# Kernel tuning notes

Hardware: AMD Instinct MI355X
Metric: run time of the kernel (lower is better)

The kernel has to match this reference:

```python
import jax, jax.numpy as jnp
import numpy as np

NUM_LAYERS = 3
N = 4096
DIM = 512
TOPK = 8
BIG = 1.0e9
EPS_COS = 1e-8
EPS_NORM = 1e-12
BN_EPS = 1e-5
LAM_K = 64.0
LAM_Z = 16.0
SIGMA_INTRA = 0.99
ALPHA = np.linspace(1.0, 1.2, NUM_LAYERS)
BETA = np.linspace(0.0, 0.0, NUM_LAYERS)


def setup_inputs() -> dict:
    key = jax.random.key(0)
    ks = jax.random.split(key, 6)
    feats = jax.random.normal(ks[0], (NUM_LAYERS, N, DIM), dtype=jnp.float32)
    labels = jax.random.randint(ks[1], (N,), 0, 64, dtype=jnp.int64)
    fc1_w = jax.random.normal(ks[2], (NUM_LAYERS, DIM, DIM), dtype=jnp.float32) * (1.0 / np.sqrt(DIM))
    fc2_w = jax.random.normal(ks[3], (NUM_LAYERS, DIM, DIM), dtype=jnp.float32) * (1.0 / np.sqrt(DIM))
    bn_gamma = jnp.ones((NUM_LAYERS, DIM), dtype=jnp.float32)
    bn_beta = jnp.zeros((NUM_LAYERS, DIM), dtype=jnp.float32)
    proj_w = jax.random.normal(ks[4], (768, DIM), dtype=jnp.float32) * (1.0 / np.sqrt(DIM))
    return {"feats": feats, "labels": labels, "fc1_w": fc1_w, "fc2_w": fc2_w,
            "bn_gamma": bn_gamma, "bn_beta": bn_beta, "proj_w": proj_w}


def _l2norm(x, axis=-1):
    return x / jnp.maximum(jnp.linalg.norm(x, axis=axis, keepdims=True), EPS_NORM)


def _pairwise_cosine(G):
    Gn = _l2norm(G)
    sim = Gn @ Gn.T
    return jnp.clip(sim, -1.0 + EPS_COS, 1.0 - EPS_COS)


def _knn_mask(sim, base_mask, topk):
    n = sim.shape[0]
    masked = (sim - BIG * jnp.eye(n, dtype=sim.dtype)) * base_mask - (1.0 - base_mask) * BIG
    k = min(topk, max(n - 1, 1))
    idx = jax.lax.top_k(masked, k)[1]  # [N, k]
    st = jnp.zeros_like(sim).at[jnp.arange(n)[:, None], idx].set(1.0)
    return jnp.maximum(st, st.T)


def _build_intra_inter(sim, labels, topk):
    same = (labels[None, :] == labels[:, None]).astype(sim.dtype)
    diff = 1.0 - same
    m_intra = _knn_mask(sim, same, topk)
    m_inter = _knn_mask(sim, diff, topk)
    sim_intra = jnp.maximum(sim * m_intra, 0.0)
    sim_inter = jnp.maximum(sim * m_inter, 0.0)
    return sim_intra, sim_inter


def _normalize_sym(sim_graph, eps=1e-8):
    d = jnp.maximum(sim_graph.sum(axis=1), eps)
    dinv = d ** -0.5
    return dinv[:, None] * sim_graph * dinv[None, :]  # == diag(dinv) @ S @ diag(dinv)


def _diffusion(K, t_diff=1):
    out = K
    for _ in range(max(t_diff - 1, 0)):
        out = out @ K
    return out


def _bn_train(x, gamma, beta):
    m = x.mean(axis=0)
    v = x.var(axis=0)  # biased, as torch BN training
    return (x - m) / jnp.sqrt(v + BN_EPS) * gamma + beta


def _gam(S, G, w1, w2, gamma, beta):
    Z = S @ (G @ w1.T)
    Z = jax.nn.relu(_bn_train(Z, gamma, beta))
    Z = S @ (Z @ w2.T)
    return Z + G


def reference(feats, labels, fc1_w, fc2_w, bn_gamma, bn_beta, proj_w):
    n = feats.shape[1]
    eye = jnp.eye(n, dtype=feats.dtype)
    same = (labels[None, :] == labels[:, None]).astype(feats.dtype)

    K_list, Z_list = [], []
    for i in range(NUM_LAYERS):
        G = feats[i]
        sim = _pairwise_cosine(G)
        sim_intra, sim_inter = _build_intra_inter(sim, labels, TOPK)
        sim_graph = float(ALPHA[i]) * sim_intra + float(BETA[i]) * sim_inter + 1e-6 * eye
        S = _normalize_sym(sim_graph)
        K = _diffusion(S, t_diff=1)
        Z = _gam(S, G, fc1_w[i], fc2_w[i], bn_gamma[i], bn_beta[i])
        K_list.append(K)
        Z_list.append(Z)

    loss_K = jnp.zeros((), dtype=feats.dtype)
    loss_Z = jnp.zeros((), dtype=feats.dtype)
    for i in range(1, NUM_LAYERS):
        K_tgt = jax.lax.stop_gradient(K_list[i])
        loss_K = loss_K + jnp.mean((K_list[i - 1] - K_tgt) ** 2)
        Zp = _l2norm(Z_list[i - 1] @ proj_w.T)
        Zc = _l2norm(Z_list[i] @ proj_w.T)
        loss_Z = loss_Z + jnp.mean((Zp - jax.lax.stop_gradient(Zc)) ** 2)

    K_idea = _diffusion(same * SIGMA_INTRA, t_diff=1)
    loss_idea = jnp.mean((K_list[-1] - K_idea) ** 2)
    return LAM_K * loss_K + LAM_Z * loss_Z + loss_idea
```

## Files before the change

kernel.cpp:

```cpp
#include <hip/hip_runtime.h>
#include <math.h>
#include <stdint.h>

#define NROWS 4096
#define DIM   512
#define NCLS  64
#define CAP   128
#define PD    768
#define NL    3
#define PARTSZ (size_t)(NCLS * 2 * 1024)

typedef __attribute__((ext_vector_type(8))) short short8v;
typedef __attribute__((ext_vector_type(4))) float f32x4;

__device__ __forceinline__ unsigned short f2bf(float f) {
  unsigned u = __float_as_uint(f);
  unsigned r = (u + 0x7FFF + ((u >> 16) & 1)) >> 16;
  return (unsigned short)r;
}

__device__ __forceinline__ void gload_lds16(const void* g, void* l) {
  auto* lp = reinterpret_cast<__attribute__((address_space(3))) unsigned int*>(
      reinterpret_cast<uintptr_t>(l));
  const auto* gp = reinterpret_cast<const __attribute__((address_space(1))) unsigned int*>(
      reinterpret_cast<uintptr_t>(g));
  __builtin_amdgcn_global_load_lds(gp, lp, 16, 0, 0);
}

__device__ __forceinline__ float waveReduce(float v) {
#pragma unroll
  for (int o = 32; o > 0; o >>= 1) v += __shfl_down(v, o);
  return v;
}

__device__ __forceinline__ float blockReduce(float v) {
  __shared__ float sh[4];
  int lane = threadIdx.x & 63, wv = threadIdx.x >> 6;
  v = waveReduce(v);
  if (lane == 0) sh[wv] = v;
  __syncthreads();
  float t = 0.f;
  if (threadIdx.x == 0) {
    int nw = (blockDim.x + 63) >> 6;
    for (int i = 0; i < nw; ++i) t += sh[i];
  }
  return t;
}

__global__ __launch_bounds__(256) void k_hist(const int* __restrict__ labels, int* __restrict__ chunkCnt) {
  __shared__ int h[NCLS];
  int t = threadIdx.x;
  if (t < NCLS) h[t] = 0;
  __syncthreads();
  atomicAdd(&h[labels[blockIdx.x * 256 + t]], 1);
  __syncthreads();
  if (t < NCLS) chunkCnt[blockIdx.x * NCLS + t] = h[t];
}

__global__ void k_scan(const int* __restrict__ chunkCnt, int* __restrict__ cnt,
                       int* __restrict__ off, int* __restrict__ chunkBase, float* __restrict__ acc) {
  __shared__ int sc[NCLS];
  int c = threadIdx.x;
  if (c < 8) acc[c] = 0.f;
  int tot = 0;
  for (int b = 0; b < 16; ++b) tot += chunkCnt[b * NCLS + c];
  cnt[c] = tot;
  sc[c] = tot;
  __syncthreads();
  if (c == 0) {
    int s = 0;
    for (int i = 0; i < NCLS; ++i) { int tv = sc[i]; sc[i] = s; s += tv; }
  }
  __syncthreads();
  int run = sc[c];
  off[c] = run;
  for (int b = 0; b < 16; ++b) { chunkBase[b * NCLS + c] = run; run += chunkCnt[b * NCLS + c]; }
  if (c == 0) off[NCLS] = NROWS;
}

__global__ __launch_bounds__(256) void k_scatter(const int* __restrict__ labels, const int* __restrict__ chunkBase,
                                                 int* __restrict__ perm, int* __restrict__ clsp) {
  __shared__ int lab[256];
  int t = threadIdx.x;
  int r = blockIdx.x * 256 + t;
  int c = labels[r];
  lab[t] = c;
  __syncthreads();
  int rank = 0;
  for (int j = 0; j < t; ++j) rank += (lab[j] == c);
  int pos = chunkBase[blockIdx.x * NCLS + c] + rank;
  perm[pos] = r;
  clsp[pos] = c;
}

__global__ __launch_bounds__(128) void k_prepw(const float* __restrict__ feats, const int* __restrict__ perm,
                                               unsigned short* __restrict__ Gpb, float* __restrict__ invn,
                                               const float4* __restrict__ fc1, const float4* __restrict__ fc2,
                                               const float4* __restrict__ proj,
                                               ushort4* __restrict__ w1, ushort4* __restrict__ w2,
                                               ushort4* __restrict__ pj, float* __restrict__ rnorm) {
  int y = blockIdx.y;
  if (y == NL) {
    const int nW = NL * DIM * DIM / 4;
    const int nP = PD * DIM / 4;
    int idx = blockIdx.x * 128 + threadIdx.x;
    const float4* src; ushort4* dst; int k;
    if (idx < nW) { src = fc1; dst = w1; k = idx; }
    else if (idx < 2 * nW) { src = fc2; dst = w2; k = idx - nW; }
    else if (idx < 2 * nW + nP) { src = proj; dst = pj; k = idx - 2 * nW; }
    else {
      int z = idx - (2 * nW + nP);
      if (z < NL * NROWS) rnorm[z] = 0.f;
      return;
    }
    float4 v = src[k];
    ushort4 o;
    o.x = f2bf(v.x); o.y = f2bf(v.y); o.z = f2bf(v.z); o.w = f2bf(v.w);
    dst[k] = o;
    return;
  }
  __shared__ float red[2];
  int l = y;
  const float* G = feats + (size_t)l * NROWS * DIM;
  unsigned short* Gp = Gpb + (size_t)l * NROWS * DIM;
  int row = blockIdx.x, t = threadIdx.x;
  const float4* src = (const float4*)(G + (size_t)perm[row] * DIM);
  float4 v = src[t];
  ushort4 b;
  b.x = f2bf(v.x); b.y = f2bf(v.y); b.z = f2bf(v.z); b.w = f2bf(v.w);
  *(ushort4*)(Gp + (size_t)row * DIM + t * 4) = b;
  float ss = v.x * v.x + v.y * v.y + v.z * v.z + v.w * v.w;
  ss = waveReduce(ss);
  if ((t & 63) == 0) red[t >> 6] = ss;
  __syncthreads();
  if (t == 0) invn[l * NROWS + row] = 1.f / fmaxf(sqrtf(red[0] + red[1]), 1e-12f);
}

__global__ __launch_bounds__(256) void k_sim(const unsigned short* __restrict__ Gpb,
                                             const float* __restrict__ invn,
                                             const int* __restrict__ cnt, const int* __restrict__ off,
                                             float* __restrict__ sim) {
  int l = blockIdx.z;
  const unsigned short* Gp = Gpb + (size_t)l * NROWS * DIM;
  const float* inv = invn + (size_t)l * NROWS;
  float* sm = sim + (size_t)l * NCLS * CAP * CAP;
  int c = blockIdx.y;
  int n = min(cnt[c], CAP);
  int ti = blockIdx.x >> 2, tj = blockIdx.x & 3;
  if (ti * 32 >= n || tj * 32 >= n) return;
  int base = off[c];
  __shared__ short As[32][40];
  __shared__ short Bs[32][40];
  const int t = threadIdx.x;
  const int lane = t & 63, wv = t >> 6;
  const int qi = wv >> 1, qj = wv & 1;
  const int fr = lane & 15, kg = lane >> 4;
  const int half = t >> 7, tt = t & 127;
  const int srow = tt >> 2, scol = (tt & 3) * 8;
  int gr = (half ? tj : ti) * 32 + srow;
  const unsigned short* ps = Gp + (size_t)(base + min(gr, n - 1)) * DIM + scol;
  short* dst = half ? &Bs[srow][scol] : &As[srow][scol];
  f32x4 acc = {};
  for (int k0 = 0; k0 < DIM; k0 += 32) {
    short8v v = *(const short8v*)(ps + k0);
    __syncthreads();
    *(short8v*)dst = v;
    __syncthreads();
    short8v af = *(const short8v*)&As[qi * 16 + fr][kg * 8];
    short8v bf = *(const short8v*)&Bs[qj * 16 + fr][kg * 8];
    acc = __builtin_amdgcn_mfma_f32_16x16x32_bf16(af, bf, acc, 0, 0, 0);
  }
  int gj = tj * 32 + qj * 16 + fr;
  int r0 = ti * 32 + qi * 16 + kg * 4;
  if (gj < n) {
    float sj = inv[base + gj];
#pragma unroll
    for (int r = 0; r < 4; ++r) {
      int gi = r0 + r;
      if (gi < n) {
        float v = acc[r] * inv[base + gi] * sj;
        v = fminf(fmaxf(v, -1.0f + 1e-8f), 1.0f - 1e-8f);
        sm[((size_t)c * CAP + gi) * CAP + gj] = v;
      }
    }
  }
}

__global__ __launch_bounds__(256) void k_topk(const float* __restrict__ sim, const int* __restrict__ cnt,
                                              const int* __restrict__ off, const int* __restrict__ clsp,
                                              int* __restrict__ t8) {
  int l = blockIdx.y;
  const float* sm = sim + (size_t)l * NCLS * CAP * CAP;
  int* t8l = t8 + (size_t)l * NROWS * 8;
  int pr = blockIdx.x * 256 + threadIdx.x;
  if (pr >= NROWS) return;
  int c = clsp[pr];
  int n = min(cnt[c], CAP);
  int loc = pr - off[c];
  const float4* row4 = (const float4*)(sm + ((size_t)c * CAP + loc) * CAP);
  float bv[8]; int bi[8];
#pragma unroll
  for (int q = 0; q < 8; ++q) { bv[q] = -3e38f; bi[q] = -1; }
  for (int j4 = 0; j4 < CAP / 4; ++j4) {
    if (j4 * 4 >= n) break;
    float4 v4 = row4[j4];
    float vv[4] = {v4.x, v4.y, v4.z, v4.w};
#pragma unroll
    for (int k = 0; k < 4; ++k) {
      int j = j4 * 4 + k;
      if (j >= n || j == loc) continue;
      float v = vv[k];
      if (v > bv[7]) {
        bv[7] = v; bi[7] = j;
#pragma unroll
        for (int q = 7; q > 0; --q) {
          if (bv[q] > bv[q - 1]) {
            float tv = bv[q]; bv[q] = bv[q - 1]; bv[q - 1] = tv;
            int tq = bi[q]; bi[q] = bi[q - 1]; bi[q - 1] = tq;
          }
        }
      }
    }
  }
#pragma unroll
  for (int q = 0; q < 8; ++q) t8l[pr * 8 + q] = bi[q];
}

__global__ __launch_bounds__(256) void k_buildS1(const float* __restrict__ sim, const int* __restrict__ cnt,
                                                 const int* __restrict__ off, const int* __restrict__ t8,
                                                 float* __restrict__ S, float* __restrict__ dinv) {
  int l = blockIdx.z;
  float alpha = 1.0f + 0.1f * l;
  const float* sm = sim + (size_t)l * NCLS * CAP * CAP;
  float* Sl = S + (size_t)l * NCLS * CAP * CAP;
  const int* t8l = t8 + (size_t)l * NROWS * 8;
  float* dv = dinv + (size_t)l * NCLS * CAP;
  int c = blockIdx.x;
  int n = min(cnt[c], CAP);
  int i0 = blockIdx.y * 32;
  if (i0 >= n) return;
  int base = off[c];
  __shared__ int sh8[CAP * 8];
  for (int i = threadIdx.x; i < n * 8; i += 256) sh8[i] = t8l[base * 8 + i];
  __syncthreads();
  int r = threadIdx.x >> 3;
  int lj = threadIdx.x & 7;
  int i = i0 + r;
  float d = 0.f;
  if (i < n) {
    int my8[8];
#pragma unroll
    for (int q = 0; q < 8; ++q) my8[q] = sh8[i * 8 + q];
    const float* srow = sm + ((size_t)c * CAP + i) * CAP;
    float* wrow = Sl + ((size_t)c * CAP + i) * CAP;
    for (int j = lj; j < n; j += 8) {
      float w;
      if (j == i) w = 1e-6f;
      else {
        bool m = false;
#pragma unroll
        for (int q = 0; q < 8; ++q) m = m || (my8[q] == j) || (sh8[j * 8 + q] == i);
        w = m ? alpha * fmaxf(srow[j], 0.f) : 0.f;
      }
      wrow[j] = w;
      d += w;
    }
  }
  d += __shfl_xor(d, 1);
  d += __shfl_xor(d, 2);
  d += __shfl_xor(d, 4);
  if (lj == 0 && i < n) dv[c * CAP + i] = 1.f / sqrtf(fmaxf(d, 1e-8f));
}

__global__ __launch_bounds__(256) void k_buildS2(float* __restrict__ S, const float* __restrict__ dinv,
                                                 const int* __restrict__ cnt) {
  int l = blockIdx.z;
  float* Sl = S + (size_t)l * NCLS * CAP * CAP;
  const float* dv = dinv + (size_t)l * NCLS * CAP;
  int c = blockIdx.x;
  int n = min(cnt[c], CAP);
  int i0 = blockIdx.y * 32;
  if (i0 >= n) return;
  __shared__ float sd[CAP];
  for (int k = threadIdx.x; k < n; k += 256) sd[k] = dv[c * CAP + k];
  __syncthreads();
  for (int p = threadIdx.x; p < 32 * CAP; p += 256) {
    int r = p >> 7, j = p & (CAP - 1);
    int i = i0 + r;
    if (i < n && j < n)
      Sl[((size_t)c * CAP + i) * CAP + j] *= sd[i] * sd[j];
  }
}

__global__ __launch_bounds__(256) void k_gemm_bf16(const short* __restrict__ A, const short* __restrict__ B,
                                                   float* __restrict__ C, float* __restrict__ rnorm, int N,
                                                   long sA, long sB, long sC) {
  int l = blockIdx.z;
  A += (size_t)l * sA; B += (size_t)l * sB; C += (size_t)l * sC;
  if (rnorm) rnorm += (size_t)l * NROWS;
  __shared__ __align__(16) short As[128][32];
  __shared__ __align__(16) short Bs[64][32];
  const int row0 = blockIdx.x * 128, col0 = blockIdx.y * 64;
  const int t = threadIdx.x;
  const int lane = t & 63, wv = t >> 6;
  const int fr = lane & 15, kg = lane >> 4;
  const int srow = lane >> 2, skb = (lane & 3) * 8;
  const short* pa = A + (size_t)(row0 + wv * 32 + srow) * DIM + skb;
  const short* pb = B + (size_t)(col0 + wv * 16 + srow) * DIM + skb;
  f32x4 acc[2][4] = {};
  for (int kt = 0; kt < DIM; kt += 32) {
    __syncthreads();
    gload_lds16(pa + kt, &As[wv * 32][0]);
    gload_lds16(pa + kt + (size_t)16 * DIM, &As[wv * 32 + 16][0]);
    gload_lds16(pb + kt, &Bs[wv * 16][0]);
    __syncthreads();
    short8v af[2], bf[4];
#pragma unroll
    for (int i = 0; i < 2; ++i) af[i] = *(const short8v*)&As[wv * 32 + i * 16 + fr][kg * 8];
#pragma unroll
    for (int j = 0; j < 4; ++j) bf[j] = *(const short8v*)&Bs[j * 16 + fr][kg * 8];
#pragma unroll
    for (int i = 0; i < 2; ++i)
#pragma unroll
      for (int j = 0; j < 4; ++j)
        acc[i][j] = __builtin_amdgcn_mfma_f32_16x16x32_bf16(af[i], bf[j], acc[i][j], 0, 0, 0);
  }
#pragma unroll
  for (int i = 0; i < 2; ++i) {
    int r0 = row0 + wv * 32 + i * 16 + kg * 4;
#pragma unroll
    for (int j = 0; j < 4; ++j) {
      int cc = col0 + j * 16 + fr;
#pragma unroll
      for (int r = 0; r < 4; ++r)
        C[(size_t)(r0 + r) * N + cc] = acc[i][j][r];
    }
    if (rnorm) {
#pragma unroll
      for (int r = 0; r < 4; ++r) {
        float ss = acc[i][0][r] * acc[i][0][r] + acc[i][1][r] * acc[i][1][r] +
                   acc[i][2][r] * acc[i][2][r] + acc[i][3][r] * acc[i][3][r];
        ss += __shfl_xor(ss, 1);
        ss += __shfl_xor(ss, 2);
        ss += __shfl_xor(ss, 4);
        ss += __shfl_xor(ss, 8);
        if (fr == 0) atomicAdd(&rnorm[r0 + r], ss);
      }
    }
  }
}

__global__ __launch_bounds__(256) void k_spmm64(const float* __restrict__ S, const float* __restrict__ X,
                                                const float* __restrict__ Gfeat, const int* __restrict__ perm,
                                                float* __restrict__ Y, unsigned short* __restrict__ Yb,
                                                float* __restrict__ part,
                                                const int* __restrict__ cnt, const int* __restrict__ off) {
  int l = blockIdx.z >> 1;
  int zc = blockIdx.z & 1;
  const float* Sl = S + (size_t)l * NCLS * CAP * CAP;
  const float4* X4 = (const float4*)(X + (size_t)l * NROWS * DIM);
  const float4* G4 = Gfeat ? (const float4*)(Gfeat + (size_t)l * NROWS * DIM) : (const float4*)nullptr;
  float4* Y4 = Y ? (float4*)(Y + (size_t)l * NROWS * DIM) : (float4*)nullptr;
  ushort4* Yb4 = Yb ? (ushort4*)(Yb + (size_t)l * NROWS * DIM) : (ushort4*)nullptr;
  int c = blockIdx.x;
  int n = min(cnt[c], CAP);
  int i0 = zc * 64;
  float* pslot = part ? part + (size_t)l * PARTSZ + (size_t)(c * 2 + zc) * 1024 : (float*)nullptr;
  __shared__ float sS[64][CAP];
  if (i0 >= n) {
    if (pslot) {
      int col = blockIdx.y * 256 + threadIdx.x;
      pslot[col] = 0.f;
      pslot[512 + col] = 0.f;
    }
    return;
  }
  int base = off[c];
  int lane = threadIdx.x & 63;
  int col4 = blockIdx.y * 64 + lane;
  int ty = threadIdx.x >> 6;
  {
    const float4* S4 = (const float4*)(Sl + ((size_t)c * CAP + i0) * CAP);
    float4* sS4 = (float4*)&sS[0][0];
    for (int idx = threadIdx.x; idx < 64 * (CAP / 4); idx += 256) {
      int r = idx >> 5;
      sS4[idx] = (i0 + r < n) ? S4[idx] : make_float4(0.f, 0.f, 0.f, 0.f);
    }
  }
  __syncthreads();
  float4 acc[16];
#pragma unroll
  for (int ii = 0; ii < 16; ++ii) acc[ii] = make_float4(0.f, 0.f, 0.f, 0.f);
  size_t xbase = (size_t)base * 128 + col4;
  int n4 = n & ~3;
  for (int j = 0; j < n4; j += 4) {
    float4 x0 = X4[xbase + (size_t)j * 128];
    float4 x1 = X4[xbase + (size_t)(j + 1) * 128];
    float4 x2 = X4[xbase + (size_t)(j + 2) * 128];
    float4 x3 = X4[xbase + (size_t)(j + 3) * 128];
#pragma unroll
    for (int ii = 0; ii < 16; ++ii) {
      float4 s4 = *(const float4*)&sS[ty * 16 + ii][j];
      acc[ii].x += s4.x * x0.x; acc[ii].y += s4.x * x0.y; acc[ii].z += s4.x * x0.z; acc[ii].w += s4.x * x0.w;
      acc[ii].x += s4.y * x1.x; acc[ii].y += s4.y * x1.y; acc[ii].z += s4.y * x1.z; acc[ii].w += s4.y * x1.w;
      acc[ii].x += s4.z * x2.x; acc[ii].y += s4.z * x2.y; acc[ii].z += s4.z * x2.z; acc[ii].w += s4.z * x2.w;
      acc[ii].x += s4.w * x3.x; acc[ii].y += s4.w * x3.y; acc[ii].z += s4.w * x3.z; acc[ii].w += s4.w * x3.w;
    }
  }
  for (int j = n4; j < n; ++j) {
    float4 x = X4[xbase + (size_t)j * 128];
#pragma unroll
    for (int ii = 0; ii < 16; ++ii) {
      float s = sS[ty * 16 + ii][j];
      acc[ii].x += s * x.x;
      acc[ii].y += s * x.y;
      acc[ii].z += s * x.z;
      acc[ii].w += s * x.w;
    }
  }
  float s1[4] = {0.f, 0.f, 0.f, 0.f}, s2[4] = {0.f, 0.f, 0.f, 0.f};
#pragma unroll
  for (int ii = 0; ii < 16; ++ii) {
    int r = i0 + ty * 16 + ii;
    if (r < n) {
      size_t o = (size_t)(base + r) * 128 + col4;
      float4 v = acc[ii];
      if (G4) {
        float4 g = G4[(size_t)perm[base + r] * 128 + col4];
        v.x += g.x; v.y += g.y; v.z += g.z; v.w += g.w;
      }
      if (pslot) {
        s1[0] += v.x; s1[1] += v.y; s1[2] += v.z; s1[3] += v.w;
        s2[0] += v.x * v.x; s2[1] += v.y * v.y; s2[2] += v.z * v.z; s2[3] += v.w * v.w;
      }
      if (Yb4) {
        ushort4 ob;
        ob.x = f2bf(v.x); ob.y = f2bf(v.y); ob.z = f2bf(v.z); ob.w = f2bf(v.w);
        Yb4[o] = ob;
      } else {
        Y4[o] = v;
      }
    }
  }
  if (pslot) {
    __syncthreads();
    float* scr = &sS[0][0];
#pragma unroll
    for (int q = 0; q < 4; ++q) {
      scr[(ty * 64 + lane) * 8 + q] = s1[q];
      scr[(ty * 64 + lane) * 8 + 4 + q] = s2[q];
    }
    __syncthreads();
    if (ty == 0) {
#pragma unroll
      for (int q = 0; q < 4; ++q) {
        float a = 0.f, b = 0.f;
#pragma unroll
        for (int g = 0; g < 4; ++g) {
          a += scr[(g * 64 + lane) * 8 + q];
          b += scr[(g * 64 + lane) * 8 + 4 + q];
        }
        int col = blockIdx.y * 256 + lane * 4 + q;
        pslot[col] = a;
        pslot[512 + col] = b;
      }
    }
  }
}

__global__ __launch_bounds__(64) void k_bnfin(const float* __restrict__ part, const float* __restrict__ gamma,
                                              const float* __restrict__ beta, float* __restrict__ sc) {
  int l = blockIdx.y;
  const float* pl = part + (size_t)l * PARTSZ;
  int k = blockIdx.x * 64 + threadIdx.x;
  float s = 0.f, s2 = 0.f;
  for (int b = 0; b < NCLS * 2; ++b) {
    s += pl[b * 1024 + k];
    s2 += pl[b * 1024 + 512 + k];
  }
  float m = s * (1.f / NROWS);
  float var = s2 * (1.f / NROWS) - m * m;
  float sg = gamma[l * DIM + k] / sqrtf(var + 1e-5f);
  sc[l * 2 * DIM + k] = sg;
  sc[l * 2 * DIM + DIM + k] = beta[l * DIM + k] - m * sg;
}

__global__ __launch_bounds__(256) void k_bnrelu(const float4* __restrict__ X, const float* __restrict__ sc,
                                                ushort4* __restrict__ Yb) {
  int l = blockIdx.y;
  const float4* Xl = X + (size_t)l * (NROWS * DIM / 4);
  const float* scl = sc + (size_t)l * 2 * DIM;
  ushort4* Yl = Yb + (size_t)l * (NROWS * DIM / 4);
  int i = blockIdx.x * blockDim.x + threadIdx.x;
  int cb = (i * 4) & (DIM - 1);
  float4 v = Xl[i];
  ushort4 o;
  o.x = f2bf(fmaxf(v.x * scl[cb + 0] + scl[DIM + cb + 0], 0.f));
  o.y = f2bf(fmaxf(v.y * scl[cb + 1] + scl[DIM + cb + 1], 0.f));
  o.z = f2bf(fmaxf(v.z * scl[cb + 2] + scl[DIM + cb + 2], 0.f));
  o.w = f2bf(fmaxf(v.w * scl[cb + 3] + scl[DIM + cb + 3], 0.f));
  Yl[i] = o;
}

__global__ __launch_bounds__(256) void k_loss(const float* __restrict__ S, const float* __restrict__ P,
                                              const float* __restrict__ rnorm, const int* __restrict__ cnt,
                                              float target, float cK, float cI, float cZ,
                                              float* __restrict__ acc) {
  int y = blockIdx.y;
  if (y < 3) {
    if (blockIdx.x >= NCLS) return;
    const float* Sa = S + (size_t)y * NCLS * CAP * CAP;
    const float* Sb = nullptr;
    float coef;
    if (y < 2) { Sb = Sa + (size_t)NCLS * CAP * CAP; coef = cK; }
    else { Sa = S + (size_t)2 * NCLS * CAP * CAP; coef = cI; }
    int c = blockIdx.x;
    int n = min(cnt[c], CAP);
    float s = 0.f;
    for (int p = threadIdx.x; p < CAP * CAP; p += 256) {
      int i = p >> 7, j = p & (CAP - 1);
      if (i < n && j < n) {
        size_t o = ((size_t)c * CAP + i) * CAP + j;
        float d = Sb ? (Sa[o] - Sb[o]) : (Sa[o] - target);
        s += d * d;
      }
    }
    s = blockReduce(s);
    if (threadIdx.x == 0) atomicAdd(acc, s * coef);
  } else {
    int yy = y - 3;
    const float* A = P + (size_t)yy * NROWS * PD;
    const float* B = A + (size_t)NROWS * PD;
    const float* rnA = rnorm + (size_t)yy * NROWS;
    const float* rnB = rnA + NROWS;
    float s = 0.f;
    int row0 = blockIdx.x * 8;
#pragma unroll
    for (int ii = 0; ii < 8; ++ii) {
      int row = row0 + ii;
      float ia = 1.f / fmaxf(sqrtf(rnA[row]), 1e-12f);
      float ib = 1.f / fmaxf(sqrtf(rnB[row]), 1e-12f);
      const float* pa = A + (size_t)row * PD;
      const float* pb = B + (size_t)row * PD;
      for (int cidx = threadIdx.x; cidx < PD; cidx += 256) {
        float d = pa[cidx] * ia - pb[cidx] * ib;
        s += d * d;
      }
    }
    s = blockReduce(s);
    if (threadIdx.x == 0) atomicAdd(acc, s * cZ);
  }
}

__global__ void k_final(const float* __restrict__ acc, float* __restrict__ out) {
  if (threadIdx.x == 0) out[0] = acc[0];
}

extern "C" void kernel_launch(void* const* d_in, const int* in_sizes, int n_in,
                              void* d_out, int out_size, void* d_ws, size_t ws_size,
                              hipStream_t stream) {
  const float* feats = (const float*)d_in[0];
  const int* labels = (const int*)d_in[1];
  const float* fc1 = (const float*)d_in[2];
  const float* fc2 = (const float*)d_in[3];
  const float* gamma = (const float*)d_in[4];
  const float* beta = (const float*)d_in[5];
  const float* proj = (const float*)d_in[6];
  float* out = (float*)d_out;

  char* w = (char*)d_ws;
  auto alloc = [&](size_t bytes) { char* p = w; w += (bytes + 255) & ~(size_t)255; return p; };
  float* bufA = (float*)alloc((size_t)NL * NROWS * DIM * 4);
  float* bufB = (float*)alloc((size_t)NL * NROWS * DIM * 4);
  unsigned short* Gpb = (unsigned short*)alloc((size_t)NL * NROWS * DIM * 2);
  unsigned short* actb = (unsigned short*)alloc((size_t)NL * NROWS * DIM * 2);
  unsigned short* W1b = (unsigned short*)alloc((size_t)NL * DIM * DIM * 2);
  unsigned short* W2b = (unsigned short*)alloc((size_t)NL * DIM * DIM * 2);
  unsigned short* Pjb = (unsigned short*)alloc((size_t)PD * DIM * 2);
  float* sim  = (float*)alloc((size_t)NL * NCLS * CAP * CAP * 4);
  float* S    = (float*)alloc((size_t)NL * NCLS * CAP * CAP * 4);
  float* P    = (float*)alloc((size_t)NL * NROWS * PD * 4);
  float* invn = (float*)alloc((size_t)NL * NROWS * 4);
  float* dinv = (float*)alloc((size_t)NL * NCLS * CAP * 4);
  float* part = (float*)alloc((size_t)NL * PARTSZ * 4);
  float* bnsc = (float*)alloc((size_t)NL * 2 * DIM * 4);
  float* rnorm = (float*)alloc((size_t)NL * NROWS * 4);
  float* acc  = (float*)alloc(256);
  int* cnt  = (int*)alloc(NCLS * 4);
  int* offc = (int*)alloc((NCLS + 1) * 4);
  int* perm = (int*)alloc(NROWS * 4);
  int* clsp = (int*)alloc(NROWS * 4);
  int* t8   = (int*)alloc((size_t)NL * NROWS * 8 * 4);
  int* chunkCnt  = (int*)alloc(16 * NCLS * 4);
  int* chunkBase = (int*)alloc(16 * NCLS * 4);

  const float LAM_K = 64.f, LAM_Z = 16.f, SIGMA = 0.99f;
  const float cK = LAM_K / ((float)NROWS * (float)NROWS);
  const float cZ = LAM_Z / ((float)NROWS * (float)PD);
  const float cI = 1.f / ((float)NROWS * (float)NROWS);
  const long sAct = (long)NROWS * DIM;
  const long sW = (long)DIM * DIM;

  hipLaunchKernelGGL(k_hist, dim3(16), dim3(256), 0, stream, labels, chunkCnt);
  hipLaunchKernelGGL(k_scan, dim3(1), dim3(64), 0, stream, chunkCnt, cnt, offc, chunkBase, acc);
  hipLaunchKernelGGL(k_scatter, dim3(16), dim3(256), 0, stream, labels, chunkBase, perm, clsp);

  hipLaunchKernelGGL(k_prepw, dim3(NROWS, NL + 1), dim3(128), 0, stream, feats, perm, Gpb, invn,
                     (const float4*)fc1, (const float4*)fc2, (const float4*)proj,
                     (ushort4*)W1b, (ushort4*)W2b, (ushort4*)Pjb, rnorm);

  hipLaunchKernelGGL(k_sim, dim3(16, NCLS, NL), dim3(256), 0, stream, Gpb, invn, cnt, offc, sim);
  hipLaunchKernelGGL(k_topk, dim3(NROWS / 256, NL), dim3(256), 0, stream, sim, cnt, offc, clsp, t8);
  hipLaunchKernelGGL(k_buildS1, dim3(NCLS, CAP / 32, NL), dim3(256), 0, stream, sim, cnt, offc, t8, S, dinv);
  hipLaunchKernelGGL(k_buildS2, dim3(NCLS, CAP / 32, NL), dim3(256), 0, stream, S, dinv, cnt);

  hipLaunchKernelGGL(k_gemm_bf16, dim3(NROWS / 128, DIM / 64, NL), dim3(256), 0, stream,
                     (const short*)Gpb, (const short*)W1b, bufA, (float*)nullptr, DIM, sAct, sW, (long)NROWS * DIM);
  hipLaunchKernelGGL(k_spmm64, dim3(NCLS, DIM / 256, 2 * NL), dim3(256), 0, stream, S, bufA,
                     (const float*)nullptr, (const int*)nullptr, bufB, (unsigned short*)nullptr, part, cnt, offc);
  hipLaunchKernelGGL(k_bnfin, dim3(DIM / 64, NL), dim3(64), 0, stream, part, gamma, beta, bnsc);
  hipLaunchKernelGGL(k_bnrelu, dim3(NROWS * DIM / 4 / 256, NL), dim3(256), 0, stream,
                     (const float4*)bufB, bnsc, (ushort4*)actb);
  hipLaunchKernelGGL(k_gemm_bf16, dim3(NROWS / 128, DIM / 64, NL), dim3(256), 0, stream,
                     (const short*)actb, (const short*)W2b, bufB, (float*)nullptr, DIM, sAct, sW, (long)NROWS * DIM);
  hipLaunchKernelGGL(k_spmm64, dim3(NCLS, DIM / 256, 2 * NL), dim3(256), 0, stream, S, bufB,
                     feats, perm, (float*)nullptr, actb, (float*)nullptr, cnt, offc);
  hipLaunchKernelGGL(k_gemm_bf16, dim3(NROWS / 128, PD / 64, NL), dim3(256), 0, stream,
                     (const short*)actb, (const short*)Pjb, P, rnorm, PD, sAct, 0L, (long)NROWS * PD);

  hipLaunchKernelGGL(k_loss, dim3(512, 5), dim3(256), 0, stream, S, P, rnorm, cnt, SIGMA, cK, cI, cZ, acc);

  hipLaunchKernelGGL(k_final, dim3(1), dim3(64), 0, stream, acc, out);
}
```

Before: 252.0 us.

## Reorder GAM as (S·X)·W with bf16 SpMM and fused BN stats in GEMM

The per-class block-diagonal SpMM now runs before each dense GEMM instead of after, reading and writing bf16 rather than fp32 activations. The GEMM epilogue takes over the residual add, bf16 output and BatchNorm sum/sumsq (via atomics), so the partial-sum buffer and the reduction loop in k_bnfin go away. This is meant to cut fp32 memory traffic and the separate stats reduction. It adds an extra bf16 rounding of S·X before the GEMM and scattered uncoalesced residual reads through perm in the epilogue.

Result: slower. 262.0 us (+4.0%).

```diff
diff --git a/kernel.cpp b/kernel.cpp
--- a/kernel.cpp
+++ b/kernel.cpp
@@ -8,7 +8,6 @@
 #define CAP   128
 #define PD    768
 #define NL    3
-#define PARTSZ (size_t)(NCLS * 2 * 1024)
 
 typedef __attribute__((ext_vector_type(8))) short short8v;
 typedef __attribute__((ext_vector_type(4))) float f32x4;
@@ -17,6 +16,15 @@
   unsigned u = __float_as_uint(f);
   unsigned r = (u + 0x7FFF + ((u >> 16) & 1)) >> 16;
   return (unsigned short)r;
+}
+
+__device__ __forceinline__ float4 bf4tof4(ushort4 u) {
+  float4 f;
+  f.x = __uint_as_float(((unsigned)u.x) << 16);
+  f.y = __uint_as_float(((unsigned)u.y) << 16);
+  f.z = __uint_as_float(((unsigned)u.z) << 16);
+  f.w = __uint_as_float(((unsigned)u.w) << 16);
+  return f;
 }
 
 __device__ __forceinline__ void gload_lds16(const void* g, void* l) {
@@ -98,7 +106,8 @@
                                                const float4* __restrict__ fc1, const float4* __restrict__ fc2,
                                                const float4* __restrict__ proj,
                                                ushort4* __restrict__ w1, ushort4* __restrict__ w2,
-                                               ushort4* __restrict__ pj, float* __restrict__ rnorm) {
+                                               ushort4* __restrict__ pj, float* __restrict__ rnorm,
+                                               float* __restrict__ bns) {
   int y = blockIdx.y;
   if (y == NL) {
     const int nW = NL * DIM * DIM / 4;
@@ -111,6 +120,7 @@
     else {
       int z = idx - (2 * nW + nP);
       if (z < NL * NROWS) rnorm[z] = 0.f;
+      else if (z < NL * NROWS + NL * 2 * DIM) bns[z - NL * NROWS] = 0.f;
       return;
     }
     float4 v = src[k];
@@ -292,12 +302,86 @@
   }
 }
 
+__global__ __launch_bounds__(256) void k_spmmb(const float* __restrict__ S, const unsigned short* __restrict__ Xb,
+                                               unsigned short* __restrict__ Ub,
+                                               const int* __restrict__ cnt, const int* __restrict__ off) {
+  int l = blockIdx.z >> 1;
+  int zc = blockIdx.z & 1;
+  const float* Sl = S + (size_t)l * NCLS * CAP * CAP;
+  const ushort4* X4 = (const ushort4*)(Xb + (size_t)l * NROWS * DIM);
+  ushort4* U4 = (ushort4*)(Ub + (size_t)l * NROWS * DIM);
+  int c = blockIdx.x;
+  int n = min(cnt[c], CAP);
+  int i0 = zc * 64;
+  if (i0 >= n) return;
+  int base = off[c];
+  int lane = threadIdx.x & 63;
+  int col4 = blockIdx.y * 64 + lane;
+  int ty = threadIdx.x >> 6;
+  __shared__ float sS[64][CAP];
+  {
+    const float4* S4 = (const float4*)(Sl + ((size_t)c * CAP + i0) * CAP);
+    float4* sS4 = (float4*)&sS[0][0];
+    for (int idx = threadIdx.x; idx < 64 * (CAP / 4); idx += 256) {
+      int r = idx >> 5;
+      sS4[idx] = (i0 + r < n) ? S4[idx] : make_float4(0.f, 0.f, 0.f, 0.f);
+    }
+  }
+  __syncthreads();
+  float4 acc[16];
+#pragma unroll
+  for (int ii = 0; ii < 16; ++ii) acc[ii] = make_float4(0.f, 0.f, 0.f, 0.f);
+  size_t xbase = (size_t)base * 128 + col4;
+  int n4 = n & ~3;
+  for (int j = 0; j < n4; j += 4) {
+    float4 x0 = bf4tof4(X4[xbase + (size_t)j * 128]);
+    float4 x1 = bf4tof4(X4[xbase + (size_t)(j + 1) * 128]);
+    float4 x2 = bf4tof4(X4[xbase + (size_t)(j + 2) * 128]);
+    float4 x3 = bf4tof4(X4[xbase + (size_t)(j + 3) * 128]);
+#pragma unroll
+    for (int ii = 0; ii < 16; ++ii) {
+      float4 s4 = *(const float4*)&sS[ty * 16 + ii][j];
+      acc[ii].x += s4.x * x0.x; acc[ii].y += s4.x * x0.y; acc[ii].z += s4.x * x0.z; acc[ii].w += s4.x * x0.w;
+      acc[ii].x += s4.y * x1.x; acc[ii].y += s4.y * x1.y; acc[ii].z += s4.y * x1.z; acc[ii].w += s4.y * x1.w;
+      acc[ii].x += s4.z * x2.x; acc[ii].y += s4.z * x2.y; acc[ii].z += s4.z * x2.z; acc[ii].w += s4.z * x2.w;
+      acc[ii].x += s4.w * x3.x; acc[ii].y += s4.w * x3.y; acc[ii].z += s4.w * x3.z; acc[ii].w += s4.w * x3.w;
+    }
+  }
+  for (int j = n4; j < n; ++j) {
+    float4 x = bf4tof4(X4[xbase + (size_t)j * 128]);
+#pragma unroll
+    for (int ii = 0; ii < 16; ++ii) {
+      float s = sS[ty * 16 + ii][j];
+      acc[ii].x += s * x.x;
+      acc[ii].y += s * x.y;
+      acc[ii].z += s * x.z;
+      acc[ii].w += s * x.w;
+    }
+  }
+#pragma unroll
+  for (int ii = 0; ii < 16; ++ii) {
+    int r = i0 + ty * 16 + ii;
+    if (r < n) {
+      ushort4 ob;
+      ob.x = f2bf(acc[ii].x); ob.y = f2bf(acc[ii].y);
+      ob.z = f2bf(acc[ii].z); ob.w = f2bf(acc[ii].w);
+      U4[(size_t)(base + r) * 128 + col4] = ob;
+    }
+  }
+}
+
 __global__ __launch_bounds__(256) void k_gemm_bf16(const short* __restrict__ A, const short* __restrict__ B,
-                                                   float* __restrict__ C, float* __restrict__ rnorm, int N,
+                                                   float* __restrict__ Cf, unsigned short* __restrict__ Cb,
+                                                   float* __restrict__ bns,
+                                                   const float* __restrict__ Gfeat, const int* __restrict__ perm,
+                                                   float* __restrict__ rnorm, int N,
                                                    long sA, long sB, long sC) {
   int l = blockIdx.z;
-  A += (size_t)l * sA; B += (size_t)l * sB; C += (size_t)l * sC;
+  A += (size_t)l * sA; B += (size_t)l * sB;
+  if (Cb) Cb += (size_t)l * sC; else Cf += (size_t)l * sC;
   if (rnorm) rnorm += (size_t)l * NROWS;
+  if (bns) bns += (size_t)l * 2 * DIM;
+  const float* Gl = Gfeat ? Gfeat + (size_t)l * NROWS * DIM : (const float*)nullptr;
   __shared__ __align__(16) short As[128][32];
   __shared__ __align__(16) short Bs[64][32];
   const int row0 = blockIdx.x * 128, col0 = blockIdx.y * 64;
@@ -325,6 +409,7 @@
       for (int j = 0; j < 4; ++j)
         acc[i][j] = __builtin_amdgcn_mfma_f32_16x16x32_bf16(af[i], bf[j], acc[i][j], 0, 0, 0);
   }
+  float st1[4] = {0.f, 0.f, 0.f, 0.f}, st2[4] = {0.f, 0.f, 0.f, 0.f};
 #pragma unroll
   for (int i = 0; i < 2; ++i) {
     int r0 = row0 + wv * 32 + i * 16 + kg * 4;
@@ -332,8 +417,13 @@
     for (int j = 0; j < 4; ++j) {
       int cc = col0 + j * 16 + fr;
 #pragma unroll
-      for (int r = 0; r < 4; ++r)
-        C[(size_t)(r0 + r) * N + cc] = acc[i][j][r];
+      for (int r = 0; r < 4; ++r) {
+        float v = acc[i][j][r];
+        if (Gl) v += Gl[(size_t)perm[r0 + r] * DIM + cc];
+        if (bns) { st1[j] += v; st2[j] += v * v; }
+        if (Cb) Cb[(size_t)(r0 + r) * N + cc] = f2bf(v);
+        else Cf[(size_t)(r0 + r) * N + cc] = v;
+      }
     }
     if (rnorm) {
 #pragma unroll
@@ -348,136 +438,27 @@
       }
     }
   }
-}
-
-__global__ __launch_bounds__(256) void k_spmm64(const float* __restrict__ S, const float* __restrict__ X,
-                                                const float* __restrict__ Gfeat, const int* __restrict__ perm,
-                                                float* __restrict__ Y, unsigned short* __restrict__ Yb,
-                                                float* __restrict__ part,
-                                                const int* __restrict__ cnt, const int* __restrict__ off) {
-  int l = blockIdx.z >> 1;
-  int zc = blockIdx.z & 1;
-  const float* Sl = S + (size_t)l * NCLS * CAP * CAP;
-  const float4* X4 = (const float4*)(X + (size_t)l * NROWS * DIM);
-  const float4* G4 = Gfeat ? (const float4*)(Gfeat + (size_t)l * NROWS * DIM) : (const float4*)nullptr;
-  float4* Y4 = Y ? (float4*)(Y + (size_t)l * NROWS * DIM) : (float4*)nullptr;
-  ushort4* Yb4 = Yb ? (ushort4*)(Yb + (size_t)l * NROWS * DIM) : (ushort4*)nullptr;
-  int c = blockIdx.x;
-  int n = min(cnt[c], CAP);
-  int i0 = zc * 64;
-  float* pslot = part ? part + (size_t)l * PARTSZ + (size_t)(c * 2 + zc) * 1024 : (float*)nullptr;
-  __shared__ float sS[64][CAP];
-  if (i0 >= n) {
-    if (pslot) {
-      int col = blockIdx.y * 256 + threadIdx.x;
-      pslot[col] = 0.f;
-      pslot[512 + col] = 0.f;
-    }
-    return;
-  }
-  int base = off[c];
-  int lane = threadIdx.x & 63;
-  int col4 = blockIdx.y * 64 + lane;
-  int ty = threadIdx.x >> 6;
-  {
-    const float4* S4 = (const float4*)(Sl + ((size_t)c * CAP + i0) * CAP);
-    float4* sS4 = (float4*)&sS[0][0];
-    for (int idx = threadIdx.x; idx < 64 * (CAP / 4); idx += 256) {
-      int r = idx >> 5;
-      sS4[idx] = (i0 + r < n) ? S4[idx] : make_float4(0.f, 0.f, 0.f, 0.f);
-    }
-  }
-  __syncthreads();
-  float4 acc[16];
-#pragma unroll
-  for (int ii = 0; ii < 16; ++ii) acc[ii] = make_float4(0.f, 0.f, 0.f, 0.f);
-  size_t xbase = (size_t)base * 128 + col4;
-  int n4 = n & ~3;
-  for (int j = 0; j < n4; j += 4) {
-    float4 x0 = X4[xbase + (size_t)j * 128];
-    float4 x1 = X4[xbase + (size_t)(j + 1) * 128];
-    float4 x2 = X4[xbase + (size_t)(j + 2) * 128];
-    float4 x3 = X4[xbase + (size_t)(j + 3) * 128];
-#pragma unroll
-    for (int ii = 0; ii < 16; ++ii) {
-      float4 s4 = *(const float4*)&sS[ty * 16 + ii][j];
-      acc[ii].x += s4.x * x0.x; acc[ii].y += s4.x * x0.y; acc[ii].z += s4.x * x0.z; acc[ii].w += s4.x * x0.w;
-      acc[ii].x += s4.y * x1.x; acc[ii].y += s4.y * x1.y; acc[ii].z += s4.y * x1.z; acc[ii].w += s4.y * x1.w;
-      acc[ii].x += s4.z * x2.x; acc[ii].y += s4.z * x2.y; acc[ii].z += s4.z * x2.z; acc[ii].w += s4.z * x2.w;
-      acc[ii].x += s4.w * x3.x; acc[ii].y += s4.w * x3.y; acc[ii].z += s4.w * x3.z; acc[ii].w += s4.w * x3.w;
-    }
-  }
-  for (int j = n4; j < n; ++j) {
-    float4 x = X4[xbase + (size_t)j * 128];
-#pragma unroll
-    for (int ii = 0; ii < 16; ++ii) {
-      float s = sS[ty * 16 + ii][j];
-      acc[ii].x += s * x.x;
-      acc[ii].y += s * x.y;
-      acc[ii].z += s * x.z;
-      acc[ii].w += s * x.w;
-    }
-  }
-  float s1[4] = {0.f, 0.f, 0.f, 0.f}, s2[4] = {0.f, 0.f, 0.f, 0.f};
-#pragma unroll
-  for (int ii = 0; ii < 16; ++ii) {
-    int r = i0 + ty * 16 + ii;
-    if (r < n) {
-      size_t o = (size_t)(base + r) * 128 + col4;
-      float4 v = acc[ii];
-      if (G4) {
-        float4 g = G4[(size_t)perm[base + r] * 128 + col4];
-        v.x += g.x; v.y += g.y; v.z += g.z; v.w += g.w;
-      }
-      if (pslot) {
-        s1[0] += v.x; s1[1] += v.y; s1[2] += v.z; s1[3] += v.w;
-        s2[0] += v.x * v.x; s2[1] += v.y * v.y; s2[2] += v.z * v.z; s2[3] += v.w * v.w;
-      }
-      if (Yb4) {
-        ushort4 ob;
-        ob.x = f2bf(v.x); ob.y = f2bf(v.y); ob.z = f2bf(v.z); ob.w = f2bf(v.w);
-        Yb4[o] = ob;
-      } else {
-        Y4[o] = v;
-      }
-    }
-  }
-  if (pslot) {
-    __syncthreads();
-    float* scr = &sS[0][0];
-#pragma unroll
-    for (int q = 0; q < 4; ++q) {
-      scr[(ty * 64 + lane) * 8 + q] = s1[q];
-      scr[(ty * 64 + lane) * 8 + 4 + q] = s2[q];
-    }
-    __syncthreads();
-    if (ty == 0) {
-#pragma unroll
-      for (int q = 0; q < 4; ++q) {
-        float a = 0.f, b = 0.f;
-#pragma unroll
-        for (int g = 0; g < 4; ++g) {
-          a += scr[(g * 64 + lane) * 8 + q];
-          b += scr[(g * 64 + lane) * 8 + 4 + q];
-        }
-        int col = blockIdx.y * 256 + lane * 4 + q;
-        pslot[col] = a;
-        pslot[512 + col] = b;
-      }
-    }
-  }
-}
-
-__global__ __launch_bounds__(64) void k_bnfin(const float* __restrict__ part, const float* __restrict__ gamma,
+  if (bns) {
+#pragma unroll
+    for (int j = 0; j < 4; ++j) {
+      float a = st1[j], b = st2[j];
+      a += __shfl_xor(a, 16); a += __shfl_xor(a, 32);
+      b += __shfl_xor(b, 16); b += __shfl_xor(b, 32);
+      if (kg == 0) {
+        int cc = col0 + j * 16 + fr;
+        atomicAdd(&bns[cc], a);
+        atomicAdd(&bns[DIM + cc], b);
+      }
+    }
+  }
+}
+
+__global__ __launch_bounds__(64) void k_bnfin(const float* __restrict__ bns, const float* __restrict__ gamma,
                                               const float* __restrict__ beta, float* __restrict__ sc) {
   int l = blockIdx.y;
-  const float* pl = part + (size_t)l * PARTSZ;
   int k = blockIdx.x * 64 + threadIdx.x;
-  float s = 0.f, s2 = 0.f;
-  for (int b = 0; b < NCLS * 2; ++b) {
-    s += pl[b * 1024 + k];
-    s2 += pl[b * 1024 + 512 + k];
-  }
+  float s = bns[l * 2 * DIM + k];
+  float s2 = bns[l * 2 * DIM + DIM + k];
   float m = s * (1.f / NROWS);
   float var = s2 * (1.f / NROWS) - m * m;
   float sg = gamma[l * DIM + k] / sqrtf(var + 1e-5f);
@@ -570,10 +551,10 @@
 
   char* w = (char*)d_ws;
   auto alloc = [&](size_t bytes) { char* p = w; w += (bytes + 255) & ~(size_t)255; return p; };
-  float* bufA = (float*)alloc((size_t)NL * NROWS * DIM * 4);
   float* bufB = (float*)alloc((size_t)NL * NROWS * DIM * 4);
   unsigned short* Gpb = (unsigned short*)alloc((size_t)NL * NROWS * DIM * 2);
   unsigned short* actb = (unsigned short*)alloc((size_t)NL * NROWS * DIM * 2);
+  unsigned short* ubuf = (unsigned short*)alloc((size_t)NL * NROWS * DIM * 2);
   unsigned short* W1b = (unsigned short*)alloc((size_t)NL * DIM * DIM * 2);
   unsigned short* W2b = (unsigned short*)alloc((size_t)NL * DIM * DIM * 2);
   unsigned short* Pjb = (unsigned short*)alloc((size_t)PD * DIM * 2);
@@ -582,7 +563,7 @@
   float* P    = (float*)alloc((size_t)NL * NROWS * PD * 4);
   float* invn = (float*)alloc((size_t)NL * NROWS * 4);
   float* dinv = (float*)alloc((size_t)NL * NCLS * CAP * 4);
-  float* part = (float*)alloc((size_t)NL * PARTSZ * 4);
+  float* bns  = (float*)alloc((size_t)NL * 2 * DIM * 4);
   float* bnsc = (float*)alloc((size_t)NL * 2 * DIM * 4);
   float* rnorm = (float*)alloc((size_t)NL * NROWS * 4);
   float* acc  = (float*)alloc(256);
@@ -607,26 +588,27 @@
 
   hipLaunchKernelGGL(k_prepw, dim3(NROWS, NL + 1), dim3(128), 0, stream, feats, perm, Gpb, invn,
                      (const float4*)fc1, (const float4*)fc2, (const float4*)proj,
-                     (ushort4*)W1b, (ushort4*)W2b, (ushort4*)Pjb, rnorm);
+                     (ushort4*)W1b, (ushort4*)W2b, (ushort4*)Pjb, rnorm, bns);
 
   hipLaunchKernelGGL(k_sim, dim3(16, NCLS, NL), dim3(256), 0, stream, Gpb, invn, cnt, offc, sim);
   hipLaunchKernelGGL(k_topk, dim3(NROWS / 256, NL), dim3(256), 0, stream, sim, cnt, offc, clsp, t8);
   hipLaunchKernelGGL(k_buildS1, dim3(NCLS, CAP / 32, NL), dim3(256), 0, stream, sim, cnt, offc, t8, S, dinv);
   hipLaunchKernelGGL(k_buildS2, dim3(NCLS, CAP / 32, NL), dim3(256), 0, stream, S, dinv, cnt);
 
+  hipLaunchKernelGGL(k_spmmb, dim3(NCLS, 2, 2 * NL), dim3(256), 0, stream, S, Gpb, ubuf, cnt, offc);
   hipLaunchKernelGGL(k_gemm_bf16, dim3(NROWS / 128, DIM / 64, NL), dim3(256), 0, stream,
-                     (const short*)Gpb, (const short*)W1b, bufA, (float*)nullptr, DIM, sAct, sW, (long)NROWS * DIM);
-  hipLaunchKernelGGL(k_spmm64, dim3(NCLS, DIM / 256, 2 * NL), dim3(256), 0, stream, S, bufA,
-                     (const float*)nullptr, (const int*)nullptr, bufB, (unsigned short*)nullptr, part, cnt, offc);
-  hipLaunchKernelGGL(k_bnfin, dim3(DIM / 64, NL), dim3(64), 0, stream, part, gamma, beta, bnsc);
+                     (const short*)ubuf, (const short*)W1b, bufB, (unsigned short*)nullptr, bns,
+                     (const float*)nullptr, (const int*)nullptr, (float*)nullptr, DIM, sAct, sW, (long)NROWS * DIM);
+  hipLaunchKernelGGL(k_bnfin, dim3(DIM / 64, NL), dim3(64), 0, stream, bns, gamma, beta, bnsc);
   hipLaunchKernelGGL(k_bnrelu, dim3(NROWS * DIM / 4 / 256, NL), dim3(256), 0, stream,
                      (const float4*)bufB, bnsc, (ushort4*)actb);
+  hipLaunchKernelGGL(k_spmmb, dim3(NCLS, 2, 2 * NL), dim3(256), 0, stream, S, actb, ubuf, cnt, offc);
   hipLaunchKernelGGL(k_gemm_bf16, dim3(NROWS / 128, DIM / 64, NL), dim3(256), 0, stream,
-                     (const short*)actb, (const short*)W2b, bufB, (float*)nullptr, DIM, sAct, sW, (long)NROWS * DIM);
-  hipLaunchKernelGGL(k_spmm64, dim3(NCLS, DIM / 256, 2 * NL), dim3(256), 0, stream, S, bufB,
-                     feats, perm, (float*)nullptr, actb, (float*)nullptr, cnt, offc);
+                     (const short*)ubuf, (const short*)W2b, (float*)nullptr, actb, (float*)nullptr,
+                     feats, perm, (float*)nullptr, DIM, sAct, sW, (long)NROWS * DIM);
   hipLaunchKernelGGL(k_gemm_bf16, dim3(NROWS / 128, PD / 64, NL), dim3(256), 0, stream,
-                     (const short*)actb, (const short*)Pjb, P, rnorm, PD, sAct, 0L, (long)NROWS * PD);
+                     (const short*)actb, (const short*)Pjb, P, (unsigned short*)nullptr, (float*)nullptr,
+                     (const float*)nullptr, (const int*)nullptr, rnorm, PD, sAct, 0L, (long)NROWS * PD);
 
   hipLaunchKernelGGL(k_loss, dim3(512, 5), dim3(256), 0, stream, S, P, rnorm, cnt, SIGMA, cK, cI, cZ, acc);
 
```
